# Performance work log

Measured on AMD Instinct MI355X. Metric: run time of the kernel, lower is better.

## Reference

```python
import jax, jax.numpy as jnp
import numpy as np

B, T, C, H = 4, 2048, 1024, 16
D = C // H  # head_dim = 64


def setup_inputs() -> dict:
    key = jax.random.key(0)
    ks = jax.random.split(key, 10)
    s = 1.0 / np.sqrt(C)
    inp = {
        "x": jax.random.normal(ks[0], (B, T, C), dtype=jnp.float32),
        "attention_mask": jnp.ones((B, T), dtype=jnp.int32),
        "Wq": jax.random.normal(ks[1], (C, C), dtype=jnp.float32) * s,
        "bq": jnp.zeros((C,), dtype=jnp.float32),
        "Wk": jax.random.normal(ks[2], (C, C), dtype=jnp.float32) * s,
        "bk": jnp.zeros((C,), dtype=jnp.float32),
        "Wv": jax.random.normal(ks[3], (C, C), dtype=jnp.float32) * s,
        "bv": jnp.zeros((C,), dtype=jnp.float32),
        "Wp": jax.random.normal(ks[4], (C, C), dtype=jnp.float32) * s,
        "bp": jnp.zeros((C,), dtype=jnp.float32),
    }
    return inp


def reference(x, attention_mask, Wq, bq, Wk, bk, Wv, bv, Wp, bp):
    # x: [B,T,C] -> q,k,v: [B,H,T,D]
    def heads(y):
        return y.reshape(B, T, H, D).transpose(0, 2, 1, 3)

    q = heads(x @ Wq + bq)
    k = heads(x @ Wk + bk)
    v = heads(x @ Wv + bv)

    scale = 1.0 / np.sqrt(D)
    att = jnp.einsum("bhqd,bhkd->bhqk", q, k) * scale  # [B,H,T,T]

    causal = jnp.tril(jnp.ones((T, T), dtype=bool))  # [T,T]
    mask = causal[None, None, :, :] & (attention_mask[:, None, None, :] != 0)
    att = jnp.where(mask, att, -jnp.inf)
    att = jax.nn.softmax(att, axis=-1)
    # dropout is identity in eval mode

    y = jnp.einsum("bhqk,bhkd->bhqd", att, v)  # [B,H,T,D]
    y = y.transpose(0, 2, 1, 3).reshape(B, T, C)
    return y @ Wp + bp
```

## Files before the change

kernel.cpp:

```cpp
#include <hip/hip_runtime.h>

#define BB 4
#define TT 2048
#define CC 1024
#define HH 16
#define DD 64

typedef unsigned short u16;
typedef unsigned int u32;
typedef __bf16 bf16;
typedef __attribute__((ext_vector_type(8))) bf16 bf16x8;
typedef __attribute__((ext_vector_type(8))) u16 u16x8;
typedef __attribute__((ext_vector_type(4))) u16 u16x4;
typedef __attribute__((ext_vector_type(4))) float f32x4;

static __device__ __forceinline__ u16 f2b(float f) {
  unsigned u = __builtin_bit_cast(unsigned, f);
  u += 0x7fffu + ((u >> 16) & 1u);
  return (u16)(u >> 16);
}
static __device__ __forceinline__ u16 bfc(float f) {
  return __builtin_bit_cast(u16, (__bf16)f);
}
static __device__ __forceinline__ float max3f(float a, float b, float c) {
  float d;
  asm("v_max3_f32 %0, %1, %2, %3" : "=v"(d) : "v"(a), "v"(b), "v"(c));
  return d;
}

__global__ __launch_bounds__(256) void prep_kernel(
    const float* __restrict__ x, const int* __restrict__ am,
    const float* __restrict__ w0, const float* __restrict__ w1,
    const float* __restrict__ w2, const float* __restrict__ w3,
    u16* __restrict__ xb, u16* __restrict__ wqkvT, u16* __restrict__ wpT,
    float* __restrict__ gm, u32* __restrict__ fwords) {
  __shared__ float t[32][33];
  const int bid = blockIdx.x, tid = threadIdx.x;
  if (bid < 4096) {
    int i = bid * 256 + tid;
    const float4* p4 = reinterpret_cast<const float4*>(x) + (size_t)i * 2;
    float4 a = p4[0], b = p4[1];
    u16x8 o;
    o[0] = f2b(a.x); o[1] = f2b(a.y); o[2] = f2b(a.z); o[3] = f2b(a.w);
    o[4] = f2b(b.x); o[5] = f2b(b.y); o[6] = f2b(b.z); o[7] = f2b(b.w);
    *reinterpret_cast<u16x8*>(xb + (size_t)i * 8) = o;
  } else if (bid < 8192) {
    int r2 = bid - 4096;
    int z = r2 >> 10, rem = r2 & 1023;
    int k0 = (rem & 31) * 32, n0 = (rem >> 5) * 32;
    const float* src = z == 0 ? w0 : z == 1 ? w1 : z == 2 ? w2 : w3;
    u16* dst = z < 3 ? wqkvT + (size_t)z * CC * CC : wpT;
    int tx = tid & 31, ty = tid >> 5;
#pragma unroll
    for (int i = 0; i < 4; ++i)
      t[ty + i * 8][tx] = src[(size_t)(k0 + ty + i * 8) * CC + n0 + tx];
    __syncthreads();
#pragma unroll
    for (int i = 0; i < 4; ++i)
      dst[(size_t)(n0 + ty + i * 8) * CC + k0 + tx] = f2b(t[tx][ty + i * 8]);
  } else {
    __shared__ u32 sf[32];
    int b = bid - 8192;
    int lane = tid & 63, w = tid >> 6;
#pragma unroll
    for (int j = 0; j < 8; ++j) {
      int c = w * 8 + j;
      int i = c * 64 + lane;
      int v = am[b * TT + i];
      gm[b * TT + i] = v ? 0.f : -1e30f;
      unsigned long long bal = __ballot(v != 0);
      if (lane == 0) sf[c] = (bal == ~0ull) ? 1u : 0u;
    }
    __syncthreads();
    if (tid == 0) {
      u32 fw = 0;
      for (int c = 0; c < 32; ++c) fw |= sf[c] << c;
      fwords[b] = fw;
    }
  }
}

__global__ __launch_bounds__(512, 2) void qkv_gemm_kernel(
    const u16* __restrict__ A, const u16* __restrict__ Bt,
    const float* __restrict__ bq, const float* __restrict__ bk, const float* __restrict__ bv,
    u16* __restrict__ q_out, u16* __restrict__ k_out, u16* __restrict__ v_out) {
  __shared__ __align__(16) char LDS[131072];
  const int tid = threadIdx.x, lane = tid & 63, w = tid >> 6;
  const int wm = w >> 2, wn = w & 3;
  const int lq = lane & 15, g = lane >> 4;
  const int m0 = blockIdx.x * 256, n0 = blockIdx.y * 256;

  const int l3 = lane >> 3;
  const int swb = ((lane & 7) ^ (l3 & 7)) * 16;

  auto LOAD_A = [&](int db, int R, int ko) {
    int rb = R + w * 8;
    __builtin_amdgcn_global_load_lds(
        (const __attribute__((address_space(1))) void*)(
            (const char*)A + (size_t)(m0 + rb + l3) * 2048 + ko + swb),
        (__attribute__((address_space(3))) void*)(LDS + db * 32768 + rb * 128), 16, 0, 0);
  };
  auto LOAD_B = [&](int db, int R, int sub, int ko) {
    int rb = R + (w >> 2) * 64 + (w & 3) * 8 + sub;
    __builtin_amdgcn_global_load_lds(
        (const __attribute__((address_space(1))) void*)(
            (const char*)Bt + (size_t)(n0 + rb + l3) * 2048 + ko + swb),
        (__attribute__((address_space(3))) void*)(LDS + 65536 + db * 32768 + rb * 128), 16, 0, 0);
  };
  auto C1 = [&](int db, int ko) { LOAD_A(db, 0, ko); LOAD_A(db, 128, ko); };
  auto C2 = [&](int db, int ko) { LOAD_B(db, 0, 0, ko); LOAD_B(db, 128, 0, ko); };
  auto C3 = [&](int db, int ko) { LOAD_B(db, 0, 32, ko); LOAD_B(db, 128, 32, ko); };
  auto C4 = [&](int db, int ko) { LOAD_A(db, 64, ko); LOAD_A(db, 192, ko); };

  const int acol0 = (g * 16) ^ ((lq & 7) << 4);
  const int acol1 = (64 + g * 16) ^ ((lq & 7) << 4);
  const int aBase = wm * 16384 + lq * 128;
  const int bBase = 65536 + wn * 8192 + lq * 128;

  f32x4 acc[8][4] = {};
  bf16x8 af[4][2], bf[2][2];

  C1(0, 0); C2(0, 0); C3(0, 0); C4(0, 0);

  for (int t = 0; t < 16; ++t) {
    const int db = t & 1, dn = db ^ 1;
    const int ko = (t + 1) * 128;
    const bool st = t < 15;
    const char* la = LDS + db * 32768 + aBase;
    const char* lb = LDS + db * 32768 + bBase;

    asm volatile("s_waitcnt vmcnt(4)" ::: "memory");
    asm volatile("s_barrier" ::: "memory");
#pragma unroll
    for (int i = 0; i < 4; ++i) {
      af[i][0] = *reinterpret_cast<const bf16x8*>(la + i * 2048 + acol0);
      af[i][1] = *reinterpret_cast<const bf16x8*>(la + i * 2048 + acol1);
    }
#pragma unroll
    for (int j = 0; j < 2; ++j) {
      bf[j][0] = *reinterpret_cast<const bf16x8*>(lb + j * 2048 + acol0);
      bf[j][1] = *reinterpret_cast<const bf16x8*>(lb + j * 2048 + acol1);
    }
    if (st) C1(dn, ko);
    asm volatile("s_waitcnt lgkmcnt(0)" ::: "memory");
    __builtin_amdgcn_sched_barrier(0);
    __builtin_amdgcn_s_setprio(1);
#pragma unroll
    for (int i = 0; i < 4; ++i)
#pragma unroll
      for (int j = 0; j < 2; ++j) {
        acc[i][j] = __builtin_amdgcn_mfma_f32_16x16x32_bf16(af[i][0], bf[j][0], acc[i][j], 0, 0, 0);
        acc[i][j] = __builtin_amdgcn_mfma_f32_16x16x32_bf16(af[i][1], bf[j][1], acc[i][j], 0, 0, 0);
      }
    __builtin_amdgcn_s_setprio(0);

    if (st) asm volatile("s_waitcnt vmcnt(4)" ::: "memory");
    else    asm volatile("s_waitcnt vmcnt(2)" ::: "memory");
    asm volatile("s_barrier" ::: "memory");
#pragma unroll
    for (int j = 0; j < 2; ++j) {
      bf[j][0] = *reinterpret_cast<const bf16x8*>(lb + (2 + j) * 2048 + acol0);
      bf[j][1] = *reinterpret_cast<const bf16x8*>(lb + (2 + j) * 2048 + acol1);
    }
    if (st) C2(dn, ko);
    asm volatile("s_waitcnt lgkmcnt(0)" ::: "memory");
    __builtin_amdgcn_sched_barrier(0);
    __builtin_amdgcn_s_setprio(1);
#pragma unroll
    for (int i = 0; i < 4; ++i)
#pragma unroll
      for (int j = 0; j < 2; ++j) {
        acc[i][2 + j] = __builtin_amdgcn_mfma_f32_16x16x32_bf16(af[i][0], bf[j][0], acc[i][2 + j], 0, 0, 0);
        acc[i][2 + j] = __builtin_amdgcn_mfma_f32_16x16x32_bf16(af[i][1], bf[j][1], acc[i][2 + j], 0, 0, 0);
      }
    __builtin_amdgcn_s_setprio(0);

    if (st) asm volatile("s_waitcnt vmcnt(4)" ::: "memory");
    else    asm volatile("s_waitcnt vmcnt(0)" ::: "memory");
    asm volatile("s_barrier" ::: "memory");
#pragma unroll
    for (int i = 0; i < 4; ++i) {
      af[i][0] = *reinterpret_cast<const bf16x8*>(la + (4 + i) * 2048 + acol0);
      af[i][1] = *reinterpret_cast<const bf16x8*>(la + (4 + i) * 2048 + acol1);
    }
#pragma unroll
    for (int j = 0; j < 2; ++j) {
      bf[j][0] = *reinterpret_cast<const bf16x8*>(lb + j * 2048 + acol0);
      bf[j][1] = *reinterpret_cast<const bf16x8*>(lb + j * 2048 + acol1);
    }
    if (st) C3(dn, ko);
    asm volatile("s_waitcnt lgkmcnt(0)" ::: "memory");
    __builtin_amdgcn_sched_barrier(0);
    __builtin_amdgcn_s_setprio(1);
#pragma unroll
    for (int i = 0; i < 4; ++i)
#pragma unroll
      for (int j = 0; j < 2; ++j) {
        acc[4 + i][j] = __builtin_amdgcn_mfma_f32_16x16x32_bf16(af[i][0], bf[j][0], acc[4 + i][j], 0, 0, 0);
        acc[4 + i][j] = __builtin_amdgcn_mfma_f32_16x16x32_bf16(af[i][1], bf[j][1], acc[4 + i][j], 0, 0, 0);
      }
    __builtin_amdgcn_s_setprio(0);

    asm volatile("s_barrier" ::: "memory");
#pragma unroll
    for (int j = 0; j < 2; ++j) {
      bf[j][0] = *reinterpret_cast<const bf16x8*>(lb + (2 + j) * 2048 + acol0);
      bf[j][1] = *reinterpret_cast<const bf16x8*>(lb + (2 + j) * 2048 + acol1);
    }
    if (st) C4(dn, ko);
    asm volatile("s_waitcnt lgkmcnt(0)" ::: "memory");
    __builtin_amdgcn_sched_barrier(0);
    __builtin_amdgcn_s_setprio(1);
#pragma unroll
    for (int i = 0; i < 4; ++i)
#pragma unroll
      for (int j = 0; j < 2; ++j) {
        acc[4 + i][2 + j] = __builtin_amdgcn_mfma_f32_16x16x32_bf16(af[i][0], bf[j][0], acc[4 + i][2 + j], 0, 0, 0);
        acc[4 + i][2 + j] = __builtin_amdgcn_mfma_f32_16x16x32_bf16(af[i][1], bf[j][1], acc[4 + i][2 + j], 0, 0, 0);
      }
    __builtin_amdgcn_s_setprio(0);
  }

  const int g3 = n0 >> 10;
  const int mrow = m0 + wm * 128;
  const int ncol = n0 + wn * 64;
  if (g3 < 2) {
    u16* dst = g3 == 0 ? q_out : k_out;
    const float* bias = g3 == 0 ? bq : bk;
    const float scl = g3 == 0 ? 0.18033688f : 1.0f;
#pragma unroll
    for (int i = 0; i < 8; ++i)
#pragma unroll
      for (int j = 0; j < 4; ++j) {
        int n = ncol + j * 16 + lq;
        int h = (n >> 6) & 15, d = n & 63;
        float bb = bias[n & 1023];
#pragma unroll
        for (int r = 0; r < 4; ++r) {
          int m = mrow + i * 16 + g * 4 + r;
          int b = m >> 11, t = m & 2047;
          dst[(((size_t)(b * HH + h)) * TT + t) * DD + d] = f2b((acc[i][j][r] + bb) * scl);
        }
      }
  } else {
#pragma unroll
    for (int i = 0; i < 8; ++i)
#pragma unroll
      for (int j = 0; j < 4; ++j) {
        int n = ncol + j * 16 + lq;
        int h = (n >> 6) & 15, d = n & 63;
        float bb = bv[n & 1023];
        int mb = mrow + i * 16 + g * 4;
        int b = mb >> 11, t = mb & 2047;
        u16x4 vv;
#pragma unroll
        for (int r = 0; r < 4; ++r) vv[r] = f2b(acc[i][j][r] + bb);
        *reinterpret_cast<u16x4*>(v_out + (((size_t)(b * HH + h)) * DD + d) * TT + t) = vv;
      }
  }
}

__global__ __launch_bounds__(256) void proj_gemm_kernel(
    const u16* __restrict__ A, const u16* __restrict__ Bt,
    const float* __restrict__ bias, float* __restrict__ f_out) {
  __shared__ __align__(16) char LDS[65536];
  const int tid = threadIdx.x, lane = tid & 63, w = tid >> 6;
  const int wm = w >> 1, wn = w & 1;
  const int lq = lane & 15, g = lane >> 4;
  const int m0 = blockIdx.x * 128, n0 = blockIdx.y * 128;
  const int l3 = lane >> 3;
  const int swb = ((lane & 7) ^ (l3 & 7)) * 16;
  f32x4 acc[4][4] = {};

  auto STAGE = [&](int db, int kt) {
    const int ko = kt * 128;
#pragma unroll
    for (int r = 0; r < 4; ++r) {
      int rb = r * 32 + w * 8;
      __builtin_amdgcn_global_load_lds(
          (const __attribute__((address_space(1))) void*)(
              (const char*)A + (size_t)(m0 + rb + l3) * 2048 + ko + swb),
          (__attribute__((address_space(3))) void*)(LDS + db * 16384 + rb * 128), 16, 0, 0);
      __builtin_amdgcn_global_load_lds(
          (const __attribute__((address_space(1))) void*)(
              (const char*)Bt + (size_t)(n0 + rb + l3) * 2048 + ko + swb),
          (__attribute__((address_space(3))) void*)(LDS + 32768 + db * 16384 + rb * 128), 16, 0, 0);
    }
  };

  const int acol0 = (g * 16) ^ ((lq & 7) << 4);
  const int acol1 = (64 + g * 16) ^ ((lq & 7) << 4);
  const int aBase = wm * 8192 + lq * 128;
  const int bBase = 32768 + wn * 8192 + lq * 128;

  STAGE(0, 0);
  STAGE(1, 1);
  for (int kt = 0; kt < 16; ++kt) {
    if (kt == 15) asm volatile("s_waitcnt vmcnt(0)" ::: "memory");
    else          asm volatile("s_waitcnt vmcnt(8)" ::: "memory");
    asm volatile("s_barrier" ::: "memory");
    const int db = kt & 1;
    const char* la = LDS + db * 16384 + aBase;
    const char* lb = LDS + db * 16384 + bBase;
    bf16x8 af[4][2], bfr[4][2];
#pragma unroll
    for (int i = 0; i < 4; ++i) {
      af[i][0] = *reinterpret_cast<const bf16x8*>(la + i * 2048 + acol0);
      af[i][1] = *reinterpret_cast<const bf16x8*>(la + i * 2048 + acol1);
      bfr[i][0] = *reinterpret_cast<const bf16x8*>(lb + i * 2048 + acol0);
      bfr[i][1] = *reinterpret_cast<const bf16x8*>(lb + i * 2048 + acol1);
    }
    asm volatile("s_waitcnt lgkmcnt(0)" ::: "memory");
    __builtin_amdgcn_sched_barrier(0);
    __builtin_amdgcn_s_setprio(1);
#pragma unroll
    for (int i = 0; i < 4; ++i)
#pragma unroll
      for (int j = 0; j < 4; ++j) {
        acc[i][j] = __builtin_amdgcn_mfma_f32_16x16x32_bf16(af[i][0], bfr[j][0], acc[i][j], 0, 0, 0);
        acc[i][j] = __builtin_amdgcn_mfma_f32_16x16x32_bf16(af[i][1], bfr[j][1], acc[i][j], 0, 0, 0);
      }
    __builtin_amdgcn_s_setprio(0);
    asm volatile("s_barrier" ::: "memory");
    if (kt + 2 < 16) STAGE(db, kt + 2);
  }

  const int mrow = m0 + wm * 64;
  const int ncol = n0 + wn * 64;
#pragma unroll
  for (int i = 0; i < 4; ++i)
#pragma unroll
    for (int j = 0; j < 4; ++j)
#pragma unroll
      for (int r = 0; r < 4; ++r) {
        int m = mrow + i * 16 + g * 4 + r;
        int n = ncol + j * 16 + lq;
        f_out[(size_t)m * CC + n] = acc[i][j][r] + bias[n];
      }
}

__global__ __launch_bounds__(256, 2) void attn_kernel(
    const u16* __restrict__ Q, const u16* __restrict__ K, const u16* __restrict__ Vt,
    const float* __restrict__ gm, const u32* __restrict__ fwords, u16* __restrict__ Y) {
  __shared__ __align__(16) char LDS[51200];
  const int flat = blockIdx.x;
  const int xcd = flat & 7, idx = flat >> 3;
  const int bh = xcd * 8 + (idx & 7);
  const int jb = 15 - (idx >> 3);
  const int b = bh >> 4, h = bh & 15;
  const int tid = threadIdx.x, lane = tid & 63, w = tid >> 6;
  const int lq = lane & 15, g = lane >> 4;
  const int qt = 4 * jb + w;
  const int q0 = qt * 32;
  const int nkt = (qt >> 1) + 1;
  const int nktm = 2 * jb + 2;
  const u32 fw = fwords[b];

  const u16* Qb = Q + (size_t)bh * TT * DD;
  const char* Kb = (const char*)(K + (size_t)bh * TT * DD);
  const char* Vb = (const char*)(Vt + (size_t)bh * DD * TT);

  const int l3 = lane >> 3, l7 = lane & 7;
  const int swb = (l7 * 16) ^ (l3 << 4);
  const char* kp0 = Kb + (2 * w + 0) * 1024 + l3 * 128 + swb;
  const char* kp1 = Kb + (2 * w + 1) * 1024 + l3 * 128 + swb;
  const char* vp0 = Vb + (size_t)((2 * w + 0) * 8 + l3) * 4096 + swb;
  const char* vp1 = Vb + (size_t)((2 * w + 1) * 8 + l3) * 4096 + swb;

  const int sw2 = (lq & 7) << 4;
  const int fb0 = lq * 128 + ((g * 16) ^ sw2);
  const int fb1 = lq * 128 + (((64) + g * 16) ^ sw2);
  const int pwb = 32768 + w * 4608 + lq * 144 + g * 8;
  const int prb = 32768 + w * 4608 + lq * 144 + g * 16;

  auto STAGE = [&](int buf, int kt2) {
    const int ko = kt2 * 8192, vo = kt2 * 128, lb = buf * 8192;
    __builtin_amdgcn_global_load_lds(
        (const __attribute__((address_space(1))) void*)(kp0 + ko),
        (__attribute__((address_space(3))) void*)(LDS + lb + (2 * w + 0) * 1024), 16, 0, 0);
    __builtin_amdgcn_global_load_lds(
        (const __attribute__((address_space(1))) void*)(kp1 + ko),
        (__attribute__((address_space(3))) void*)(LDS + lb + (2 * w + 1) * 1024), 16, 0, 0);
    __builtin_amdgcn_global_load_lds(
        (const __attribute__((address_space(1))) void*)(vp0 + vo),
        (__attribute__((address_space(3))) void*)(LDS + 16384 + lb + (2 * w + 0) * 1024), 16, 0, 0);
    __builtin_amdgcn_global_load_lds(
        (const __attribute__((address_space(1))) void*)(vp1 + vo),
        (__attribute__((address_space(3))) void*)(LDS + 16384 + lb + (2 * w + 1) * 1024), 16, 0, 0);
  };

  bf16x8 qf[2][2];
#pragma unroll
  for (int n = 0; n < 2; ++n)
#pragma unroll
    for (int ks = 0; ks < 2; ++ks)
      qf[n][ks] = *reinterpret_cast<const bf16x8*>(
          Qb + (size_t)(q0 + n * 16 + lq) * DD + ks * 32 + g * 8);

  const u16x8 onesu = {0x3F80, 0x3F80, 0x3F80, 0x3F80, 0x3F80, 0x3F80, 0x3F80, 0x3F80};
  const bf16x8 ones = __builtin_bit_cast(bf16x8, onesu);

  f32x4 o[4][2] = {};
  f32x4 l_acc[2] = {};
  float mrun[2] = {-1e30f, -1e30f};
  const f32x4 z4 = {0.f, 0.f, 0.f, 0.f};

  STAGE(0, 0);
  STAGE(1, 1);

  auto TILE = [&](int BUF, int kt) {
    if (kt < nktm - 1)
      asm volatile("s_waitcnt vmcnt(4)" ::: "memory");
    else
      asm volatile("s_waitcnt vmcnt(0)" ::: "memory");
    asm volatile("s_barrier" ::: "memory");

    if (kt < nkt) {
      const int kv0 = kt * 64;
      bf16x8 kf0[4], kf1[4];
#pragma unroll
      for (int m = 0; m < 4; ++m) {
        kf0[m] = *reinterpret_cast<const bf16x8*>(LDS + BUF * 8192 + m * 2048 + fb0);
        kf1[m] = *reinterpret_cast<const bf16x8*>(LDS + BUF * 8192 + m * 2048 + fb1);
      }
      f32x4 s[4][2];
      __builtin_amdgcn_s_setprio(1);
#pragma unroll
      for (int m = 0; m < 4; ++m)
#pragma unroll
        for (int n = 0; n < 2; ++n) {
          s[m][n] = __builtin_amdgcn_mfma_f32_16x16x32_bf16(kf0[m], qf[n][0], z4, 0, 0, 0);
          s[m][n] = __builtin_amdgcn_mfma_f32_16x16x32_bf16(kf1[m], qf[n][1], s[m][n], 0, 0, 0);
        }
      __builtin_amdgcn_s_setprio(0);

      if (!((fw >> kt) & 1u)) {
#pragma unroll
        for (int m = 0; m < 4; ++m) {
          float4 mv = *reinterpret_cast<const float4*>(gm + b * TT + kv0 + m * 16 + g * 4);
#pragma unroll
          for (int n = 0; n < 2; ++n) {
            s[m][n][0] += mv.x; s[m][n][1] += mv.y;
            s[m][n][2] += mv.z; s[m][n][3] += mv.w;
          }
        }
      }
      if (kt == nkt - 1) {
#pragma unroll
        for (int n = 0; n < 2; ++n) {
          const int q = q0 + n * 16 + lq;
#pragma unroll
          for (int m = 0; m < 4; ++m)
#pragma unroll
            for (int r = 0; r < 4; ++r) {
              int kv = kv0 + m * 16 + g * 4 + r;
              s[m][n][r] = (kv <= q) ? s[m][n][r] : -1e30f;
            }
        }
      }

#pragma unroll
      for (int n = 0; n < 2; ++n) {
        float m1 = max3f(s[0][n][0], s[0][n][1], s[0][n][2]);
        float m2 = max3f(s[0][n][3], s[1][n][0], s[1][n][1]);
        float m3 = max3f(s[1][n][2], s[1][n][3], s[2][n][0]);
        float m4 = max3f(s[2][n][1], s[2][n][2], s[2][n][3]);
        float m5 = max3f(s[3][n][0], s[3][n][1], s[3][n][2]);
        float rm = fmaxf(max3f(m1, m2, m3), max3f(m4, m5, s[3][n][3]));
        if (!__all(rm <= mrun[n] + 8.f)) {
          float rg = fmaxf(rm, __shfl_xor(rm, 16));
          rg = fmaxf(rg, __shfl_xor(rg, 32));
          float mnew = fmaxf(mrun[n], rg);
          float corr = __builtin_exp2f(mrun[n] - mnew);
          mrun[n] = mnew;
          l_acc[n] *= corr;
#pragma unroll
          for (int nd = 0; nd < 4; ++nd)
#pragma unroll
            for (int r = 0; r < 4; ++r) o[nd][n][r] *= corr;
        }
        const float mn = mrun[n];
#pragma unroll
        for (int m = 0; m < 4; ++m) {
          float p0 = __builtin_exp2f(s[m][n][0] - mn);
          float p1 = __builtin_exp2f(s[m][n][1] - mn);
          float p2 = __builtin_exp2f(s[m][n][2] - mn);
          float p3 = __builtin_exp2f(s[m][n][3] - mn);
          u32 wa, wb;
          asm("v_cvt_pk_bf16_f32 %0, %1, %2" : "=v"(wa) : "v"(p0), "v"(p1));
          asm("v_cvt_pk_bf16_f32 %0, %1, %2" : "=v"(wb) : "v"(p2), "v"(p3));
          uint2 pw; pw.x = wa; pw.y = wb;
          *reinterpret_cast<uint2*>(LDS + pwb + n * 2304 + m * 32) = pw;
        }
      }

      asm volatile("s_waitcnt lgkmcnt(0)" ::: "memory");
      __builtin_amdgcn_sched_barrier(0);

      __builtin_amdgcn_s_setprio(1);
#pragma unroll
      for (int ks = 0; ks < 2; ++ks) {
        const int fb = ks ? fb1 : fb0;
        bf16x8 pf0 = *reinterpret_cast<const bf16x8*>(LDS + prb + 0 * 2304 + ks * 64);
        bf16x8 pf1 = *reinterpret_cast<const bf16x8*>(LDS + prb + 1 * 2304 + ks * 64);
#pragma unroll
        for (int nd = 0; nd < 4; ++nd) {
          bf16x8 vf = *reinterpret_cast<const bf16x8*>(LDS + 16384 + BUF * 8192 + nd * 2048 + fb);
          o[nd][0] = __builtin_amdgcn_mfma_f32_16x16x32_bf16(vf, pf0, o[nd][0], 0, 0, 0);
          o[nd][1] = __builtin_amdgcn_mfma_f32_16x16x32_bf16(vf, pf1, o[nd][1], 0, 0, 0);
        }
        l_acc[0] = __builtin_amdgcn_mfma_f32_16x16x32_bf16(ones, pf0, l_acc[0], 0, 0, 0);
        l_acc[1] = __builtin_amdgcn_mfma_f32_16x16x32_bf16(ones, pf1, l_acc[1], 0, 0, 0);
      }
      __builtin_amdgcn_s_setprio(0);
    }

    asm volatile("s_barrier" ::: "memory");
    if (kt + 2 < nktm) STAGE(BUF, kt + 2);
  };

  for (int kt = 0; kt < nktm; kt += 2) {
    TILE(0, kt);
    TILE(1, kt + 1);
  }

#pragma unroll
  for (int n = 0; n < 2; ++n) {
    float inv = 1.0f / l_acc[n][0];
    const int q = q0 + n * 16 + lq;
#pragma unroll
    for (int nd = 0; nd < 4; ++nd) {
      u16x4 yv;
#pragma unroll
      for (int r = 0; r < 4; ++r) yv[r] = bfc(o[nd][n][r] * inv);
      *reinterpret_cast<u16x4*>(
          Y + ((size_t)(b * TT + q)) * CC + h * DD + nd * 16 + g * 4) = yv;
    }
  }
}

extern "C" void kernel_launch(void* const* d_in, const int* in_sizes, int n_in,
                              void* d_out, int out_size, void* d_ws, size_t ws_size,
                              hipStream_t stream) {
  const float* x  = (const float*)d_in[0];
  const int*   am = (const int*)d_in[1];
  const float* Wq = (const float*)d_in[2];
  const float* bq = (const float*)d_in[3];
  const float* Wk = (const float*)d_in[4];
  const float* bk = (const float*)d_in[5];
  const float* Wv = (const float*)d_in[6];
  const float* bv = (const float*)d_in[7];
  const float* Wp = (const float*)d_in[8];
  const float* bp = (const float*)d_in[9];
  float* out = (float*)d_out;

  char* ws = (char*)d_ws;
  u16* xb    = (u16*)(ws);
  u16* wqkvT = (u16*)(ws + (16ull << 20));
  u16* wpT   = (u16*)(ws + (22ull << 20));
  u16* qw    = (u16*)(ws + (24ull << 20));
  u16* kw    = (u16*)(ws + (40ull << 20));
  u16* vw    = (u16*)(ws + (56ull << 20));
  u16* yb    = (u16*)(ws + (72ull << 20));
  float* gm  = (float*)d_out;
  u32* fwords = (u32*)((char*)d_out + (64ull << 10));

  prep_kernel<<<dim3(8196), 256, 0, stream>>>(
      x, am, Wq, Wk, Wv, Wp, xb, wqkvT, wpT, gm, fwords);
  qkv_gemm_kernel<<<dim3(32, 12), 512, 0, stream>>>(
      xb, wqkvT, bq, bk, bv, qw, kw, vw);
  attn_kernel<<<dim3(1024), 256, 0, stream>>>(qw, kw, vw, gm, fwords, yb);
  proj_gemm_kernel<<<dim3(64, 8), 256, 0, stream>>>(yb, wpT, bp, out);
}
```

Baseline: 167.8 us.

## Shrink QKV GEMM tiles and widen attention blocks to eight waves

```diff
diff --git a/kernel.cpp b/kernel.cpp
--- a/kernel.cpp
+++ b/kernel.cpp
@@ -80,156 +80,81 @@
   }
 }
 
-__global__ __launch_bounds__(512, 2) void qkv_gemm_kernel(
+__global__ __launch_bounds__(256) void qkv_gemm_kernel(
     const u16* __restrict__ A, const u16* __restrict__ Bt,
     const float* __restrict__ bq, const float* __restrict__ bk, const float* __restrict__ bv,
     u16* __restrict__ q_out, u16* __restrict__ k_out, u16* __restrict__ v_out) {
-  __shared__ __align__(16) char LDS[131072];
+  __shared__ __align__(16) char LDS[65536];
   const int tid = threadIdx.x, lane = tid & 63, w = tid >> 6;
-  const int wm = w >> 2, wn = w & 3;
+  const int wm = w >> 1, wn = w & 1;
   const int lq = lane & 15, g = lane >> 4;
-  const int m0 = blockIdx.x * 256, n0 = blockIdx.y * 256;
-
+  const int m0 = blockIdx.x * 128, n0 = blockIdx.y * 128;
   const int l3 = lane >> 3;
   const int swb = ((lane & 7) ^ (l3 & 7)) * 16;
-
-  auto LOAD_A = [&](int db, int R, int ko) {
-    int rb = R + w * 8;
-    __builtin_amdgcn_global_load_lds(
-        (const __attribute__((address_space(1))) void*)(
-            (const char*)A + (size_t)(m0 + rb + l3) * 2048 + ko + swb),
-        (__attribute__((address_space(3))) void*)(LDS + db * 32768 + rb * 128), 16, 0, 0);
+  f32x4 acc[4][4] = {};
+
+  auto STAGE = [&](int db, int kt) {
+    const int ko = kt * 128;
+#pragma unroll
+    for (int r = 0; r < 4; ++r) {
+      int rb = r * 32 + w * 8;
+      __builtin_amdgcn_global_load_lds(
+          (const __attribute__((address_space(1))) void*)(
+              (const char*)A + (size_t)(m0 + rb + l3) * 2048 + ko + swb),
+          (__attribute__((address_space(3))) void*)(LDS + db * 16384 + rb * 128), 16, 0, 0);
+      __builtin_amdgcn_global_load_lds(
+          (const __attribute__((address_space(1))) void*)(
+              (const char*)Bt + (size_t)(n0 + rb + l3) * 2048 + ko + swb),
+          (__attribute__((address_space(3))) void*)(LDS + 32768 + db * 16384 + rb * 128), 16, 0, 0);
+    }
   };
-  auto LOAD_B = [&](int db, int R, int sub, int ko) {
-    int rb = R + (w >> 2) * 64 + (w & 3) * 8 + sub;
-    __builtin_amdgcn_global_load_lds(
-        (const __attribute__((address_space(1))) void*)(
-            (const char*)Bt + (size_t)(n0 + rb + l3) * 2048 + ko + swb),
-        (__attribute__((address_space(3))) void*)(LDS + 65536 + db * 32768 + rb * 128), 16, 0, 0);
-  };
-  auto C1 = [&](int db, int ko) { LOAD_A(db, 0, ko); LOAD_A(db, 128, ko); };
-  auto C2 = [&](int db, int ko) { LOAD_B(db, 0, 0, ko); LOAD_B(db, 128, 0, ko); };
-  auto C3 = [&](int db, int ko) { LOAD_B(db, 0, 32, ko); LOAD_B(db, 128, 32, ko); };
-  auto C4 = [&](int db, int ko) { LOAD_A(db, 64, ko); LOAD_A(db, 192, ko); };
 
   const int acol0 = (g * 16) ^ ((lq & 7) << 4);
   const int acol1 = (64 + g * 16) ^ ((lq & 7) << 4);
-  const int aBase = wm * 16384 + lq * 128;
-  const int bBase = 65536 + wn * 8192 + lq * 128;
-
-  f32x4 acc[8][4] = {};
-  bf16x8 af[4][2], bf[2][2];
-
-  C1(0, 0); C2(0, 0); C3(0, 0); C4(0, 0);
-
-  for (int t = 0; t < 16; ++t) {
-    const int db = t & 1, dn = db ^ 1;
-    const int ko = (t + 1) * 128;
-    const bool st = t < 15;
-    const char* la = LDS + db * 32768 + aBase;
-    const char* lb = LDS + db * 32768 + bBase;
-
-    asm volatile("s_waitcnt vmcnt(4)" ::: "memory");
-    asm volatile("s_barrier" ::: "memory");
+  const int aBase = wm * 8192 + lq * 128;
+  const int bBase = 32768 + wn * 8192 + lq * 128;
+
+  STAGE(0, 0);
+  STAGE(1, 1);
+  for (int kt = 0; kt < 16; ++kt) {
+    if (kt == 15) asm volatile("s_waitcnt vmcnt(0)" ::: "memory");
+    else          asm volatile("s_waitcnt vmcnt(8)" ::: "memory");
+    asm volatile("s_barrier" ::: "memory");
+    const int db = kt & 1;
+    const char* la = LDS + db * 16384 + aBase;
+    const char* lb = LDS + db * 16384 + bBase;
+    bf16x8 af[4][2], bfr[4][2];
 #pragma unroll
     for (int i = 0; i < 4; ++i) {
       af[i][0] = *reinterpret_cast<const bf16x8*>(la + i * 2048 + acol0);
       af[i][1] = *reinterpret_cast<const bf16x8*>(la + i * 2048 + acol1);
-    }
-#pragma unroll
-    for (int j = 0; j < 2; ++j) {
-      bf[j][0] = *reinterpret_cast<const bf16x8*>(lb + j * 2048 + acol0);
-      bf[j][1] = *reinterpret_cast<const bf16x8*>(lb + j * 2048 + acol1);
-    }
-    if (st) C1(dn, ko);
+      bfr[i][0] = *reinterpret_cast<const bf16x8*>(lb + i * 2048 + acol0);
+      bfr[i][1] = *reinterpret_cast<const bf16x8*>(lb + i * 2048 + acol1);
+    }
     asm volatile("s_waitcnt lgkmcnt(0)" ::: "memory");
     __builtin_amdgcn_sched_barrier(0);
     __builtin_amdgcn_s_setprio(1);
 #pragma unroll
     for (int i = 0; i < 4; ++i)
 #pragma unroll
-      for (int j = 0; j < 2; ++j) {
-        acc[i][j] = __builtin_amdgcn_mfma_f32_16x16x32_bf16(af[i][0], bf[j][0], acc[i][j], 0, 0, 0);
-        acc[i][j] = __builtin_amdgcn_mfma_f32_16x16x32_bf16(af[i][1], bf[j][1], acc[i][j], 0, 0, 0);
+      for (int j = 0; j < 4; ++j) {
+        acc[i][j] = __builtin_amdgcn_mfma_f32_16x16x32_bf16(af[i][0], bfr[j][0], acc[i][j], 0, 0, 0);
+        acc[i][j] = __builtin_amdgcn_mfma_f32_16x16x32_bf16(af[i][1], bfr[j][1], acc[i][j], 0, 0, 0);
       }
     __builtin_amdgcn_s_setprio(0);
-
-    if (st) asm volatile("s_waitcnt vmcnt(4)" ::: "memory");
-    else    asm volatile("s_waitcnt vmcnt(2)" ::: "memory");
-    asm volatile("s_barrier" ::: "memory");
-#pragma unroll
-    for (int j = 0; j < 2; ++j) {
-      bf[j][0] = *reinterpret_cast<const bf16x8*>(lb + (2 + j) * 2048 + acol0);
-      bf[j][1] = *reinterpret_cast<const bf16x8*>(lb + (2 + j) * 2048 + acol1);
-    }
-    if (st) C2(dn, ko);
-    asm volatile("s_waitcnt lgkmcnt(0)" ::: "memory");
-    __builtin_amdgcn_sched_barrier(0);
-    __builtin_amdgcn_s_setprio(1);
-#pragma unroll
-    for (int i = 0; i < 4; ++i)
-#pragma unroll
-      for (int j = 0; j < 2; ++j) {
-        acc[i][2 + j] = __builtin_amdgcn_mfma_f32_16x16x32_bf16(af[i][0], bf[j][0], acc[i][2 + j], 0, 0, 0);
-        acc[i][2 + j] = __builtin_amdgcn_mfma_f32_16x16x32_bf16(af[i][1], bf[j][1], acc[i][2 + j], 0, 0, 0);
-      }
-    __builtin_amdgcn_s_setprio(0);
-
-    if (st) asm volatile("s_waitcnt vmcnt(4)" ::: "memory");
-    else    asm volatile("s_waitcnt vmcnt(0)" ::: "memory");
-    asm volatile("s_barrier" ::: "memory");
-#pragma unroll
-    for (int i = 0; i < 4; ++i) {
-      af[i][0] = *reinterpret_cast<const bf16x8*>(la + (4 + i) * 2048 + acol0);
-      af[i][1] = *reinterpret_cast<const bf16x8*>(la + (4 + i) * 2048 + acol1);
-    }
-#pragma unroll
-    for (int j = 0; j < 2; ++j) {
-      bf[j][0] = *reinterpret_cast<const bf16x8*>(lb + j * 2048 + acol0);
-      bf[j][1] = *reinterpret_cast<const bf16x8*>(lb + j * 2048 + acol1);
-    }
-    if (st) C3(dn, ko);
-    asm volatile("s_waitcnt lgkmcnt(0)" ::: "memory");
-    __builtin_amdgcn_sched_barrier(0);
-    __builtin_amdgcn_s_setprio(1);
-#pragma unroll
-    for (int i = 0; i < 4; ++i)
-#pragma unroll
-      for (int j = 0; j < 2; ++j) {
-        acc[4 + i][j] = __builtin_amdgcn_mfma_f32_16x16x32_bf16(af[i][0], bf[j][0], acc[4 + i][j], 0, 0, 0);
-        acc[4 + i][j] = __builtin_amdgcn_mfma_f32_16x16x32_bf16(af[i][1], bf[j][1], acc[4 + i][j], 0, 0, 0);
-      }
-    __builtin_amdgcn_s_setprio(0);
-
-    asm volatile("s_barrier" ::: "memory");
-#pragma unroll
-    for (int j = 0; j < 2; ++j) {
-      bf[j][0] = *reinterpret_cast<const bf16x8*>(lb + (2 + j) * 2048 + acol0);
-      bf[j][1] = *reinterpret_cast<const bf16x8*>(lb + (2 + j) * 2048 + acol1);
-    }
-    if (st) C4(dn, ko);
-    asm volatile("s_waitcnt lgkmcnt(0)" ::: "memory");
-    __builtin_amdgcn_sched_barrier(0);
-    __builtin_amdgcn_s_setprio(1);
-#pragma unroll
-    for (int i = 0; i < 4; ++i)
-#pragma unroll
-      for (int j = 0; j < 2; ++j) {
-        acc[4 + i][2 + j] = __builtin_amdgcn_mfma_f32_16x16x32_bf16(af[i][0], bf[j][0], acc[4 + i][2 + j], 0, 0, 0);
-        acc[4 + i][2 + j] = __builtin_amdgcn_mfma_f32_16x16x32_bf16(af[i][1], bf[j][1], acc[4 + i][2 + j], 0, 0, 0);
-      }
-    __builtin_amdgcn_s_setprio(0);
+    asm volatile("s_barrier" ::: "memory");
+    if (kt + 2 < 16) STAGE(db, kt + 2);
   }
 
   const int g3 = n0 >> 10;
-  const int mrow = m0 + wm * 128;
+  const int mrow = m0 + wm * 64;
   const int ncol = n0 + wn * 64;
   if (g3 < 2) {
     u16* dst = g3 == 0 ? q_out : k_out;
     const float* bias = g3 == 0 ? bq : bk;
     const float scl = g3 == 0 ? 0.18033688f : 1.0f;
 #pragma unroll
-    for (int i = 0; i < 8; ++i)
+    for (int i = 0; i < 4; ++i)
 #pragma unroll
       for (int j = 0; j < 4; ++j) {
         int n = ncol + j * 16 + lq;
@@ -244,7 +169,7 @@
       }
   } else {
 #pragma unroll
-    for (int i = 0; i < 8; ++i)
+    for (int i = 0; i < 4; ++i)
 #pragma unroll
       for (int j = 0; j < 4; ++j) {
         int n = ncol + j * 16 + lq;
@@ -339,21 +264,21 @@
       }
 }
 
-__global__ __launch_bounds__(256, 2) void attn_kernel(
+__global__ __launch_bounds__(512, 4) void attn_kernel(
     const u16* __restrict__ Q, const u16* __restrict__ K, const u16* __restrict__ Vt,
     const float* __restrict__ gm, const u32* __restrict__ fwords, u16* __restrict__ Y) {
-  __shared__ __align__(16) char LDS[51200];
+  __shared__ __align__(16) char LDS[69632];
   const int flat = blockIdx.x;
   const int xcd = flat & 7, idx = flat >> 3;
   const int bh = xcd * 8 + (idx & 7);
-  const int jb = 15 - (idx >> 3);
+  const int jb = 7 - (idx >> 3);
   const int b = bh >> 4, h = bh & 15;
   const int tid = threadIdx.x, lane = tid & 63, w = tid >> 6;
   const int lq = lane & 15, g = lane >> 4;
-  const int qt = 4 * jb + w;
+  const int qt = 8 * jb + w;
   const int q0 = qt * 32;
   const int nkt = (qt >> 1) + 1;
-  const int nktm = 2 * jb + 2;
+  const int nktm = 4 * jb + 4;
   const u32 fw = fwords[b];
 
   const u16* Qb = Q + (size_t)bh * TT * DD;
@@ -362,10 +287,8 @@
 
   const int l3 = lane >> 3, l7 = lane & 7;
   const int swb = (l7 * 16) ^ (l3 << 4);
-  const char* kp0 = Kb + (2 * w + 0) * 1024 + l3 * 128 + swb;
-  const char* kp1 = Kb + (2 * w + 1) * 1024 + l3 * 128 + swb;
-  const char* vp0 = Vb + (size_t)((2 * w + 0) * 8 + l3) * 4096 + swb;
-  const char* vp1 = Vb + (size_t)((2 * w + 1) * 8 + l3) * 4096 + swb;
+  const char* kp = Kb + w * 1024 + l3 * 128 + swb;
+  const char* vp = Vb + (size_t)(w * 8 + l3) * 4096 + swb;
 
   const int sw2 = (lq & 7) << 4;
   const int fb0 = lq * 128 + ((g * 16) ^ sw2);
@@ -376,17 +299,11 @@
   auto STAGE = [&](int buf, int kt2) {
     const int ko = kt2 * 8192, vo = kt2 * 128, lb = buf * 8192;
     __builtin_amdgcn_global_load_lds(
-        (const __attribute__((address_space(1))) void*)(kp0 + ko),
-        (__attribute__((address_space(3))) void*)(LDS + lb + (2 * w + 0) * 1024), 16, 0, 0);
+        (const __attribute__((address_space(1))) void*)(kp + ko),
+        (__attribute__((address_space(3))) void*)(LDS + lb + w * 1024), 16, 0, 0);
     __builtin_amdgcn_global_load_lds(
-        (const __attribute__((address_space(1))) void*)(kp1 + ko),
-        (__attribute__((address_space(3))) void*)(LDS + lb + (2 * w + 1) * 1024), 16, 0, 0);
-    __builtin_amdgcn_global_load_lds(
-        (const __attribute__((address_space(1))) void*)(vp0 + vo),
-        (__attribute__((address_space(3))) void*)(LDS + 16384 + lb + (2 * w + 0) * 1024), 16, 0, 0);
-    __builtin_amdgcn_global_load_lds(
-        (const __attribute__((address_space(1))) void*)(vp1 + vo),
-        (__attribute__((address_space(3))) void*)(LDS + 16384 + lb + (2 * w + 1) * 1024), 16, 0, 0);
+        (const __attribute__((address_space(1))) void*)(vp + vo),
+        (__attribute__((address_space(3))) void*)(LDS + 16384 + lb + w * 1024), 16, 0, 0);
   };
 
   bf16x8 qf[2][2];
@@ -410,7 +327,7 @@
 
   auto TILE = [&](int BUF, int kt) {
     if (kt < nktm - 1)
-      asm volatile("s_waitcnt vmcnt(4)" ::: "memory");
+      asm volatile("s_waitcnt vmcnt(2)" ::: "memory");
     else
       asm volatile("s_waitcnt vmcnt(0)" ::: "memory");
     asm volatile("s_barrier" ::: "memory");
@@ -567,8 +484,8 @@
 
   prep_kernel<<<dim3(8196), 256, 0, stream>>>(
       x, am, Wq, Wk, Wv, Wp, xb, wqkvT, wpT, gm, fwords);
-  qkv_gemm_kernel<<<dim3(32, 12), 512, 0, stream>>>(
+  qkv_gemm_kernel<<<dim3(64, 24), 256, 0, stream>>>(
       xb, wqkvT, bq, bk, bv, qw, kw, vw);
-  attn_kernel<<<dim3(1024), 256, 0, stream>>>(qw, kw, vw, gm, fwords, yb);
+  attn_kernel<<<dim3(512), 512, 0, stream>>>(qw, kw, vw, gm, fwords, yb);
   proj_gemm_kernel<<<dim3(64, 8), 256, 0, stream>>>(yb, wpT, bp, out);
 }
```

New measurement: 168.0 us. No clear change (+0.2%).

## Restructure QKV GEMM pipeline to keep B fragments in registers and prefetch deeper

Applied to the files above, without the earlier changes.

```diff
diff --git a/kernel.cpp b/kernel.cpp
--- a/kernel.cpp
+++ b/kernel.cpp
@@ -80,7 +80,7 @@
   }
 }
 
-__global__ __launch_bounds__(512, 2) void qkv_gemm_kernel(
+__global__ __launch_bounds__(512, 1) void qkv_gemm_kernel(
     const u16* __restrict__ A, const u16* __restrict__ Bt,
     const float* __restrict__ bq, const float* __restrict__ bk, const float* __restrict__ bv,
     u16* __restrict__ q_out, u16* __restrict__ k_out, u16* __restrict__ v_out) {
@@ -89,48 +89,57 @@
   const int wm = w >> 2, wn = w & 3;
   const int lq = lane & 15, g = lane >> 4;
   const int m0 = blockIdx.x * 256, n0 = blockIdx.y * 256;
-
   const int l3 = lane >> 3;
   const int swb = ((lane & 7) ^ (l3 & 7)) * 16;
 
-  auto LOAD_A = [&](int db, int R, int ko) {
-    int rb = R + w * 8;
-    __builtin_amdgcn_global_load_lds(
-        (const __attribute__((address_space(1))) void*)(
-            (const char*)A + (size_t)(m0 + rb + l3) * 2048 + ko + swb),
-        (__attribute__((address_space(3))) void*)(LDS + db * 32768 + rb * 128), 16, 0, 0);
+  const char* pA[4];
+  const char* pB[4];
+#pragma unroll
+  for (int h = 0; h < 2; ++h)
+#pragma unroll
+    for (int r = 0; r < 2; ++r) {
+      int row = h * 128 + r * 64 + w * 8;
+      pA[h * 2 + r] = (const char*)A + (size_t)(m0 + row + l3) * 2048 + swb;
+      pB[h * 2 + r] = (const char*)Bt + (size_t)(n0 + row + l3) * 2048 + swb;
+    }
+
+  auto SA = [&](int db, int h, int t) {
+    const int ko = t * 128;
+#pragma unroll
+    for (int r = 0; r < 2; ++r)
+      __builtin_amdgcn_global_load_lds(
+          (const __attribute__((address_space(1))) void*)(pA[h * 2 + r] + ko),
+          (__attribute__((address_space(3))) void*)(
+              LDS + db * 32768 + h * 16384 + r * 8192 + w * 1024), 16, 0, 0);
   };
-  auto LOAD_B = [&](int db, int R, int sub, int ko) {
-    int rb = R + (w >> 2) * 64 + (w & 3) * 8 + sub;
-    __builtin_amdgcn_global_load_lds(
-        (const __attribute__((address_space(1))) void*)(
-            (const char*)Bt + (size_t)(n0 + rb + l3) * 2048 + ko + swb),
-        (__attribute__((address_space(3))) void*)(LDS + 65536 + db * 32768 + rb * 128), 16, 0, 0);
+  auto SB = [&](int db, int h, int t) {
+    const int ko = t * 128;
+#pragma unroll
+    for (int r = 0; r < 2; ++r)
+      __builtin_amdgcn_global_load_lds(
+          (const __attribute__((address_space(1))) void*)(pB[h * 2 + r] + ko),
+          (__attribute__((address_space(3))) void*)(
+              LDS + 65536 + db * 32768 + h * 16384 + r * 8192 + w * 1024), 16, 0, 0);
   };
-  auto C1 = [&](int db, int ko) { LOAD_A(db, 0, ko); LOAD_A(db, 128, ko); };
-  auto C2 = [&](int db, int ko) { LOAD_B(db, 0, 0, ko); LOAD_B(db, 128, 0, ko); };
-  auto C3 = [&](int db, int ko) { LOAD_B(db, 0, 32, ko); LOAD_B(db, 128, 32, ko); };
-  auto C4 = [&](int db, int ko) { LOAD_A(db, 64, ko); LOAD_A(db, 192, ko); };
 
   const int acol0 = (g * 16) ^ ((lq & 7) << 4);
   const int acol1 = (64 + g * 16) ^ ((lq & 7) << 4);
   const int aBase = wm * 16384 + lq * 128;
-  const int bBase = 65536 + wn * 8192 + lq * 128;
+  const int bBase = 65536 + (wn >> 1) * 16384 + ((wn & 1) * 64 + lq) * 128;
 
   f32x4 acc[8][4] = {};
-  bf16x8 af[4][2], bf[2][2];
-
-  C1(0, 0); C2(0, 0); C3(0, 0); C4(0, 0);
+  bf16x8 af[4][2], bn01[2][2], bn23[2][2];
+
+  SA(0, 0, 0); SA(0, 1, 0); SB(0, 0, 0); SB(0, 1, 0);
+  SB(1, 0, 1); SB(1, 1, 1);
+  asm volatile("s_waitcnt vmcnt(4)" ::: "memory");
+  asm volatile("s_barrier" ::: "memory");
 
   for (int t = 0; t < 16; ++t) {
     const int db = t & 1, dn = db ^ 1;
-    const int ko = (t + 1) * 128;
-    const bool st = t < 15;
     const char* la = LDS + db * 32768 + aBase;
     const char* lb = LDS + db * 32768 + bBase;
 
-    asm volatile("s_waitcnt vmcnt(4)" ::: "memory");
-    asm volatile("s_barrier" ::: "memory");
 #pragma unroll
     for (int i = 0; i < 4; ++i) {
       af[i][0] = *reinterpret_cast<const bf16x8*>(la + i * 2048 + acol0);
@@ -138,10 +147,11 @@
     }
 #pragma unroll
     for (int j = 0; j < 2; ++j) {
-      bf[j][0] = *reinterpret_cast<const bf16x8*>(lb + j * 2048 + acol0);
-      bf[j][1] = *reinterpret_cast<const bf16x8*>(lb + j * 2048 + acol1);
-    }
-    if (st) C1(dn, ko);
+      bn01[j][0] = *reinterpret_cast<const bf16x8*>(lb + j * 2048 + acol0);
+      bn01[j][1] = *reinterpret_cast<const bf16x8*>(lb + j * 2048 + acol1);
+    }
+    if (t + 1 < 16) SA(dn, 0, t + 1);
+    asm volatile("s_barrier" ::: "memory");
     asm volatile("s_waitcnt lgkmcnt(0)" ::: "memory");
     __builtin_amdgcn_sched_barrier(0);
     __builtin_amdgcn_s_setprio(1);
@@ -149,20 +159,19 @@
     for (int i = 0; i < 4; ++i)
 #pragma unroll
       for (int j = 0; j < 2; ++j) {
-        acc[i][j] = __builtin_amdgcn_mfma_f32_16x16x32_bf16(af[i][0], bf[j][0], acc[i][j], 0, 0, 0);
-        acc[i][j] = __builtin_amdgcn_mfma_f32_16x16x32_bf16(af[i][1], bf[j][1], acc[i][j], 0, 0, 0);
+        acc[i][j] = __builtin_amdgcn_mfma_f32_16x16x32_bf16(af[i][0], bn01[j][0], acc[i][j], 0, 0, 0);
+        acc[i][j] = __builtin_amdgcn_mfma_f32_16x16x32_bf16(af[i][1], bn01[j][1], acc[i][j], 0, 0, 0);
       }
     __builtin_amdgcn_s_setprio(0);
-
-    if (st) asm volatile("s_waitcnt vmcnt(4)" ::: "memory");
-    else    asm volatile("s_waitcnt vmcnt(2)" ::: "memory");
-    asm volatile("s_barrier" ::: "memory");
+    asm volatile("s_barrier" ::: "memory");
+
 #pragma unroll
     for (int j = 0; j < 2; ++j) {
-      bf[j][0] = *reinterpret_cast<const bf16x8*>(lb + (2 + j) * 2048 + acol0);
-      bf[j][1] = *reinterpret_cast<const bf16x8*>(lb + (2 + j) * 2048 + acol1);
-    }
-    if (st) C2(dn, ko);
+      bn23[j][0] = *reinterpret_cast<const bf16x8*>(lb + (2 + j) * 2048 + acol0);
+      bn23[j][1] = *reinterpret_cast<const bf16x8*>(lb + (2 + j) * 2048 + acol1);
+    }
+    if (t + 1 < 16) SA(dn, 1, t + 1);
+    asm volatile("s_barrier" ::: "memory");
     asm volatile("s_waitcnt lgkmcnt(0)" ::: "memory");
     __builtin_amdgcn_sched_barrier(0);
     __builtin_amdgcn_s_setprio(1);
@@ -170,25 +179,19 @@
     for (int i = 0; i < 4; ++i)
 #pragma unroll
       for (int j = 0; j < 2; ++j) {
-        acc[i][2 + j] = __builtin_amdgcn_mfma_f32_16x16x32_bf16(af[i][0], bf[j][0], acc[i][2 + j], 0, 0, 0);
-        acc[i][2 + j] = __builtin_amdgcn_mfma_f32_16x16x32_bf16(af[i][1], bf[j][1], acc[i][2 + j], 0, 0, 0);
+        acc[i][2 + j] = __builtin_amdgcn_mfma_f32_16x16x32_bf16(af[i][0], bn23[j][0], acc[i][2 + j], 0, 0, 0);
+        acc[i][2 + j] = __builtin_amdgcn_mfma_f32_16x16x32_bf16(af[i][1], bn23[j][1], acc[i][2 + j], 0, 0, 0);
       }
     __builtin_amdgcn_s_setprio(0);
-
-    if (st) asm volatile("s_waitcnt vmcnt(4)" ::: "memory");
-    else    asm volatile("s_waitcnt vmcnt(0)" ::: "memory");
-    asm volatile("s_barrier" ::: "memory");
+    asm volatile("s_barrier" ::: "memory");
+
 #pragma unroll
     for (int i = 0; i < 4; ++i) {
       af[i][0] = *reinterpret_cast<const bf16x8*>(la + (4 + i) * 2048 + acol0);
       af[i][1] = *reinterpret_cast<const bf16x8*>(la + (4 + i) * 2048 + acol1);
     }
-#pragma unroll
-    for (int j = 0; j < 2; ++j) {
-      bf[j][0] = *reinterpret_cast<const bf16x8*>(lb + j * 2048 + acol0);
-      bf[j][1] = *reinterpret_cast<const bf16x8*>(lb + j * 2048 + acol1);
-    }
-    if (st) C3(dn, ko);
+    if (t + 2 < 16) SB(db, 0, t + 2);
+    asm volatile("s_barrier" ::: "memory");
     asm volatile("s_waitcnt lgkmcnt(0)" ::: "memory");
     __builtin_amdgcn_sched_barrier(0);
     __builtin_amdgcn_s_setprio(1);
@@ -196,29 +199,26 @@
     for (int i = 0; i < 4; ++i)
 #pragma unroll
       for (int j = 0; j < 2; ++j) {
-        acc[4 + i][j] = __builtin_amdgcn_mfma_f32_16x16x32_bf16(af[i][0], bf[j][0], acc[4 + i][j], 0, 0, 0);
-        acc[4 + i][j] = __builtin_amdgcn_mfma_f32_16x16x32_bf16(af[i][1], bf[j][1], acc[4 + i][j], 0, 0, 0);
+        acc[4 + i][j] = __builtin_amdgcn_mfma_f32_16x16x32_bf16(af[i][0], bn01[j][0], acc[4 + i][j], 0, 0, 0);
+        acc[4 + i][j] = __builtin_amdgcn_mfma_f32_16x16x32_bf16(af[i][1], bn01[j][1], acc[4 + i][j], 0, 0, 0);
       }
     __builtin_amdgcn_s_setprio(0);
-
-    asm volatile("s_barrier" ::: "memory");
-#pragma unroll
-    for (int j = 0; j < 2; ++j) {
-      bf[j][0] = *reinterpret_cast<const bf16x8*>(lb + (2 + j) * 2048 + acol0);
-      bf[j][1] = *reinterpret_cast<const bf16x8*>(lb + (2 + j) * 2048 + acol1);
-    }
-    if (st) C4(dn, ko);
-    asm volatile("s_waitcnt lgkmcnt(0)" ::: "memory");
-    __builtin_amdgcn_sched_barrier(0);
+    asm volatile("s_barrier" ::: "memory");
+
+    if (t < 14) asm volatile("s_waitcnt vmcnt(2)" ::: "memory");
+    else        asm volatile("s_waitcnt vmcnt(0)" ::: "memory");
+    if (t + 2 < 16) SB(db, 1, t + 2);
+    asm volatile("s_barrier" ::: "memory");
     __builtin_amdgcn_s_setprio(1);
 #pragma unroll
     for (int i = 0; i < 4; ++i)
 #pragma unroll
       for (int j = 0; j < 2; ++j) {
-        acc[4 + i][2 + j] = __builtin_amdgcn_mfma_f32_16x16x32_bf16(af[i][0], bf[j][0], acc[4 + i][2 + j], 0, 0, 0);
-        acc[4 + i][2 + j] = __builtin_amdgcn_mfma_f32_16x16x32_bf16(af[i][1], bf[j][1], acc[4 + i][2 + j], 0, 0, 0);
+        acc[4 + i][2 + j] = __builtin_amdgcn_mfma_f32_16x16x32_bf16(af[i][0], bn23[j][0], acc[4 + i][2 + j], 0, 0, 0);
+        acc[4 + i][2 + j] = __builtin_amdgcn_mfma_f32_16x16x32_bf16(af[i][1], bn23[j][1], acc[4 + i][2 + j], 0, 0, 0);
       }
     __builtin_amdgcn_s_setprio(0);
+    asm volatile("s_barrier" ::: "memory");
   }
 
   const int g3 = n0 >> 10;
```

Result: no change. 168.9 us (+0.7%).
